# Kernel optimization log

Hardware: AMD Instinct MI355X
Metric: run time of the kernel (lower is better)

## Reference

```python
import jax, jax.numpy as jnp
import numpy as np

B, P, D, A = 256, 196, 512, 512

def setup_inputs() -> dict:
    key = jax.random.key(0)
    ks = jax.random.split(key, 12)
    sc = 1.0 / np.sqrt(D)
    sa = 1.0 / np.sqrt(A)
    return {
        "encoder_out": jax.random.normal(ks[0], (B, P, D), jnp.float32),
        "decoder_hidden": jax.random.normal(ks[1], (B, D), jnp.float32),
        "st": jax.random.normal(ks[2], (B, D), jnp.float32),
        "Wv": jax.random.normal(ks[3], (D, A), jnp.float32) * sc,
        "bv": jnp.zeros((A,), jnp.float32),
        "Wh": jax.random.normal(ks[4], (D, A), jnp.float32) * sc,
        "bh": jnp.zeros((A,), jnp.float32),
        "Ws": jax.random.normal(ks[5], (D, A), jnp.float32) * sc,
        "bs": jnp.zeros((A,), jnp.float32),
        "Wav": jax.random.normal(ks[6], (A,), jnp.float32) * sa,
        "bav": jnp.zeros((), jnp.float32),
        "Was": jax.random.normal(ks[7], (A,), jnp.float32) * sa,
        "bas": jnp.zeros((), jnp.float32),
    }

def reference(encoder_out, decoder_hidden, st, Wv, bv, Wh, bh, Ws, bs, Wav, bav, Was, bas):
    # hidden: (B, A)
    hidden = decoder_hidden @ Wh + bh
    # v: (B, P, A)
    v = jnp.einsum('bpd,da->bpa', encoder_out, Wv) + bv
    # z_t: (B, P) -- additive attention scores over pixels
    z_t = jnp.einsum('bpa,a->bp', jnp.tanh(v + hidden[:, None, :]), Wav) + bav
    alpha_t = jax.nn.softmax(z_t, axis=1)
    # c_t: (B, D) -- attention-weighted encoding
    c_t = jnp.einsum('bpd,bp->bd', encoder_out, alpha_t)
    # sentinel branch: s (B, A), s_att (B, 1)
    s = st @ Ws + bs
    s_att = jnp.tanh(s + hidden) @ Was + bas  # (B,)
    z_t_extended = jnp.concatenate([z_t, s_att[:, None]], axis=1)  # (B, P+1)
    alpha_t_hat = jax.nn.softmax(z_t_extended, axis=1)
    beta_t = alpha_t_hat[:, -1:]  # (B, 1)
    c_hat_t = beta_t * st + (1.0 - beta_t) * c_t
    return (c_hat_t, alpha_t, beta_t)
```

## Files before the change

kernel.cpp:

```cpp
#include <hip/hip_runtime.h>
#include <hip/hip_bf16.h>
#include <cstdint>

#define B_ 256
#define P_ 196
#define D_ 512
#define A_ 512

#define OUT_CHAT  0
#define OUT_ALPHA (B_*D_)
#define OUT_BETA  (B_*D_ + B_*P_)

typedef unsigned short ushort_t;
typedef uint32_t u32;
typedef uint64_t u64;
typedef __attribute__((ext_vector_type(8))) __bf16 bf16x8;
typedef __attribute__((ext_vector_type(4))) float f32x4;

__device__ __forceinline__ ushort_t f2bf(float f) {
    union { float f; u32 i; } v; v.f = f;
    u32 r = (v.i + 0x7fffu + ((v.i >> 16) & 1u)) >> 16;
    return (ushort_t)r;
}
__device__ __forceinline__ float bfbits2f(u32 lo16) {
    union { u32 i; float f; } v; v.i = lo16 << 16; return v.f;
}
__device__ __forceinline__ u32 cvt2bf(float x, float y) {
    union { __hip_bfloat162 h; u32 u; } v;
    v.h = __float22bfloat162_rn(make_float2(x, y));
    return v.u;
}
__device__ __forceinline__ float tanh_fast(float x) {
    float e = __expf(2.0f * x);
    return 1.0f - 2.0f / (e + 1.0f);
}
__device__ __forceinline__ void async_load16(const ushort_t* g, ushort_t* l) {
    __builtin_amdgcn_global_load_lds(
        (const __attribute__((address_space(1))) unsigned int*)g,
        (__attribute__((address_space(3))) unsigned int*)l, 16, 0, 0);
}

__global__ __launch_bounds__(256) void k_prep(
    const float* __restrict__ E, const float* __restrict__ dh,
    const float* __restrict__ st,
    const float* __restrict__ Wv, const float* __restrict__ Wh,
    const float* __restrict__ Ws,
    ushort_t* __restrict__ Ebf, ushort_t* __restrict__ dhbf,
    ushort_t* __restrict__ stbf,
    ushort_t* __restrict__ WvT, ushort_t* __restrict__ WhT,
    ushort_t* __restrict__ WsT)
{
    __shared__ ushort_t tile[32][33];
    int bx = blockIdx.x;
    if (bx < 12544) {
        size_t i0 = (size_t)bx * 512 + threadIdx.x;
        const float4* src = (const float4*)E;
        u64* dst = (u64*)Ebf;
        float4 v0 = src[i0];
        float4 v1 = src[i0 + 256];
        dst[i0]       = (u64)cvt2bf(v0.x, v0.y) | ((u64)cvt2bf(v0.z, v0.w) << 32);
        dst[i0 + 256] = (u64)cvt2bf(v1.x, v1.y) | ((u64)cvt2bf(v1.z, v1.w) << 32);
    } else if (bx < 12672) {
        int gid = (bx - 12544) * 256 + threadIdx.x;
        float4 dv = ((const float4*)dh)[gid];
        float4 sv = ((const float4*)st)[gid];
        ((u64*)dhbf)[gid] = (u64)cvt2bf(dv.x, dv.y) | ((u64)cvt2bf(dv.z, dv.w) << 32);
        ((u64*)stbf)[gid] = (u64)cvt2bf(sv.x, sv.y) | ((u64)cvt2bf(sv.z, sv.w) << 32);
    } else {
        int idx = bx - 12672;
        int z   = idx >> 8;
        int rem = idx & 255;
        int tby = rem >> 4, tbx = rem & 15;
        const float* W  = (z == 0) ? Wv  : (z == 1) ? Wh  : Ws;
        ushort_t*    WT = (z == 0) ? WvT : (z == 1) ? WhT : WsT;
        int t = threadIdx.x, r = t >> 5, c = t & 31;
#pragma unroll
        for (int i = 0; i < 4; ++i) {
            int row = r + 8 * i;
            tile[row][c] = f2bf(W[(size_t)(tby * 32 + row) * A_ + tbx * 32 + c]);
        }
        __syncthreads();
#pragma unroll
        for (int i = 0; i < 4; ++i) {
            int row = r + 8 * i;
            WT[(size_t)(tbx * 32 + row) * D_ + tby * 32 + c] = tile[c][row];
        }
    }
}

#define PADK 72

__global__ __launch_bounds__(256) void k1_mfma(
    const ushort_t* __restrict__ dhbf, const ushort_t* __restrict__ stbf,
    const ushort_t* __restrict__ WhT,  const ushort_t* __restrict__ WsT,
    const float* __restrict__ bh, const float* __restrict__ bs,
    float* __restrict__ hidden_ws, float* __restrict__ s_ws)
{
    __shared__ ushort_t As[128 * PADK];
    __shared__ ushort_t Bs[128 * PADK];

    int mat = blockIdx.z;
    const ushort_t* Abf = mat ? stbf : dhbf;
    const ushort_t* WT  = mat ? WsT  : WhT;
    const float*    bia = mat ? bs   : bh;
    float*          outp = mat ? s_ws : hidden_ws;

    int tid = threadIdx.x;
    int m0 = blockIdx.y * 128;
    int n0 = blockIdx.x * 128;

    int lane = tid & 63, w = tid >> 6;
    int wm = w & 1, wn = w >> 1;
    int col = lane & 15, q = lane >> 4;

    f32x4 acc[4][4];
#pragma unroll
    for (int tm = 0; tm < 4; ++tm)
#pragma unroll
        for (int tn = 0; tn < 4; ++tn)
            acc[tm][tn] = (f32x4){0.f, 0.f, 0.f, 0.f};

    const ushort_t* arow = As + (wm * 64 + col) * PADK + q * 8;
    const ushort_t* brow = Bs + (wn * 64 + col) * PADK + q * 8;

    int sr = tid >> 3, sc = tid & 7;
    for (int kt = 0; kt < D_ / 64; ++kt) {
#pragma unroll
        for (int i = 0; i < 4; ++i) {
            int row = sr + i * 32;
            *(uint4*)(As + row * PADK + sc * 8) =
                *(const uint4*)(Abf + (size_t)(m0 + row) * D_ + kt * 64 + sc * 8);
            *(uint4*)(Bs + row * PADK + sc * 8) =
                *(const uint4*)(WT + (size_t)(n0 + row) * D_ + kt * 64 + sc * 8);
        }
        __syncthreads();
#pragma unroll
        for (int ks = 0; ks < 2; ++ks) {
            bf16x8 afr[4];
#pragma unroll
            for (int tm = 0; tm < 4; ++tm)
                afr[tm] = *(const bf16x8*)(arow + tm * 16 * PADK + ks * 32);
#pragma unroll
            for (int tn = 0; tn < 4; ++tn) {
                bf16x8 bfr = *(const bf16x8*)(brow + tn * 16 * PADK + ks * 32);
#pragma unroll
                for (int tm = 0; tm < 4; ++tm)
                    acc[tm][tn] = __builtin_amdgcn_mfma_f32_16x16x32_bf16(
                        afr[tm], bfr, acc[tm][tn], 0, 0, 0);
            }
        }
        __syncthreads();
    }

#pragma unroll
    for (int tm = 0; tm < 4; ++tm)
#pragma unroll
        for (int r = 0; r < 4; ++r) {
            int b = m0 + wm * 64 + tm * 16 + q * 4 + r;
#pragma unroll
            for (int tn = 0; tn < 4; ++tn) {
                int n = n0 + wn * 64 + tn * 16 + col;
                outp[(size_t)b * A_ + n] = acc[tm][tn][r] + bia[n];
            }
        }
}

#define BM 128
#define BN 256
#define BKk 64
__global__ __launch_bounds__(256, 3) void k2_z_bf(
    const ushort_t* __restrict__ Ebf, const ushort_t* __restrict__ WvT,
    const float* __restrict__ hidden_ws, const float* __restrict__ bv,
    const float* __restrict__ Wav, float* __restrict__ z2_ws)
{
    __shared__ ushort_t As[BM * BKk];
    __shared__ ushort_t Bs[BN * BKk];
    __shared__ float hv_s[2][BN];
    __shared__ float wav_s[BN];
    __shared__ float zpart[2][BM];

    int tid = threadIdx.x;
    int m0  = blockIdx.x * BM;
    int n0  = blockIdx.y * BN;
    int b0  = m0 / P_;
    int b1  = (m0 + BM - 1) / P_;

    {
        int a = n0 + tid;
        float bva = bv[a];
        hv_s[0][tid] = hidden_ws[(size_t)b0 * A_ + a] + bva;
        hv_s[1][tid] = hidden_ws[(size_t)b1 * A_ + a] + bva;
        wav_s[tid]   = Wav[a];
    }

    int lane = tid & 63, w = tid >> 6;
    int wm = w & 1, wn = w >> 1;
    int col = lane & 15, q = lane >> 4;

    f32x4 acc[4][8];
#pragma unroll
    for (int tm = 0; tm < 4; ++tm)
#pragma unroll
        for (int tn = 0; tn < 8; ++tn)
            acc[tm][tn] = (f32x4){0.f, 0.f, 0.f, 0.f};

    int srow = tid >> 3, spos = tid & 7;
    int gch  = spos ^ (srow & 7);
    const ushort_t* agb = Ebf + (size_t)(m0 + srow) * D_ + gch * 8;
    const ushort_t* bgb = WvT + (size_t)(n0 + srow) * D_ + gch * 8;
    ushort_t* alb = As + tid * 8;
    ushort_t* blb = Bs + tid * 8;

    int fx = col & 7;

    for (int kt = 0; kt < D_ / BKk; ++kt) {
#pragma unroll
        for (int i = 0; i < 4; ++i)
            async_load16(agb + (size_t)i * 32 * D_ + kt * BKk, alb + i * 2048);
#pragma unroll
        for (int i = 0; i < 8; ++i)
            async_load16(bgb + (size_t)i * 32 * D_ + kt * BKk, blb + i * 2048);
        __syncthreads();
#pragma unroll
        for (int ks = 0; ks < 2; ++ks) {
            bf16x8 afr[4];
#pragma unroll
            for (int tm = 0; tm < 4; ++tm)
                afr[tm] = *(const bf16x8*)(As + (wm * 64 + tm * 16 + col) * BKk
                                              + (((ks * 4 + q) ^ fx) * 8));
#pragma unroll
            for (int tn = 0; tn < 8; ++tn) {
                bf16x8 bfr = *(const bf16x8*)(Bs + (wn * 128 + tn * 16 + col) * BKk
                                                 + (((ks * 4 + q) ^ fx) * 8));
#pragma unroll
                for (int tm = 0; tm < 4; ++tm)
                    acc[tm][tn] = __builtin_amdgcn_mfma_f32_16x16x32_bf16(
                        afr[tm], bfr, acc[tm][tn], 0, 0, 0);
            }
        }
        __syncthreads();
    }

#pragma unroll
    for (int tm = 0; tm < 4; ++tm) {
#pragma unroll
        for (int r = 0; r < 4; ++r) {
            int row = wm * 64 + tm * 16 + q * 4 + r;
            int m   = m0 + row;
            int bsel = (m / P_) - b0;
            float zr = 0.f;
#pragma unroll
            for (int tn = 0; tn < 8; ++tn) {
                int nl = wn * 128 + tn * 16 + col;
                zr += wav_s[nl] * tanh_fast(acc[tm][tn][r] + hv_s[bsel][nl]);
            }
#pragma unroll
            for (int msk = 1; msk < 16; msk <<= 1)
                zr += __shfl_xor(zr, msk, 64);
            if (col == 0) zpart[wn][row] = zr;
        }
    }
    __syncthreads();
    if (tid < BM)
        z2_ws[(size_t)blockIdx.y * (B_ * P_) + m0 + tid] =
            zpart[0][tid] + zpart[1][tid];
}

__global__ __launch_bounds__(256) void k3_softmax(
    const float* __restrict__ z2_ws, const float* __restrict__ hidden_ws,
    const float* __restrict__ s_ws, const float* __restrict__ Was,
    const float* __restrict__ bas, const float* __restrict__ bav,
    float* __restrict__ alpha_ws, float* __restrict__ beta_ws,
    float* __restrict__ out)
{
    __shared__ float red[4];
    __shared__ float bm_s, bl_s, sa_s;
    int b = blockIdx.x, t = threadIdx.x;

    {
        int a0 = t, a1 = t + 256;
        float part = Was[a0] * tanh_fast(s_ws[(size_t)b * A_ + a0] + hidden_ws[(size_t)b * A_ + a0])
                   + Was[a1] * tanh_fast(s_ws[(size_t)b * A_ + a1] + hidden_ws[(size_t)b * A_ + a1]);
#pragma unroll
        for (int o = 32; o >= 1; o >>= 1) part += __shfl_down(part, o, 64);
        if ((t & 63) == 0) red[t >> 6] = part;
        __syncthreads();
        if (t == 0) sa_s = red[0] + red[1] + red[2] + red[3] + bas[0];
        __syncthreads();
    }

    float zv = (t < P_) ? (z2_ws[(size_t)b * P_ + t]
                         + z2_ws[(size_t)(B_ * P_) + (size_t)b * P_ + t] + bav[0])
                        : -1e30f;

    float m = zv;
#pragma unroll
    for (int o = 32; o >= 1; o >>= 1) m = fmaxf(m, __shfl_xor(m, o, 64));
    if ((t & 63) == 0) red[t >> 6] = m;
    __syncthreads();
    if (t == 0) bm_s = fmaxf(fmaxf(red[0], red[1]), fmaxf(red[2], red[3]));
    __syncthreads();
    float m1 = bm_s;

    float e = (t < P_) ? __expf(zv - m1) : 0.f;
    float s = e;
#pragma unroll
    for (int o = 32; o >= 1; o >>= 1) s += __shfl_xor(s, o, 64);
    if ((t & 63) == 0) red[t >> 6] = s;
    __syncthreads();
    if (t == 0) bl_s = red[0] + red[1] + red[2] + red[3];
    __syncthreads();
    float l1 = bl_s;

    if (t < P_) {
        float alpha = e / l1;
        alpha_ws[(size_t)b * P_ + t] = alpha;
        out[OUT_ALPHA + (size_t)b * P_ + t] = alpha;
    }
    float sa = sa_s;
    float m2 = fmaxf(m1, sa);
    float l2 = __expf(m1 - m2) * l1 + __expf(sa - m2);
    float beta = __expf(sa - m2) / l2;
    if (t == 0) {
        beta_ws[b] = beta;
        out[OUT_BETA + b] = beta;
    }
}

__global__ __launch_bounds__(256) void k4_final(
    const ushort_t* __restrict__ Ebf, const float* __restrict__ st,
    const float* __restrict__ alpha_ws, const float* __restrict__ beta_ws,
    float* __restrict__ out)
{
    __shared__ float al[P_];
    int b = blockIdx.x, t = threadIdx.x;
    if (t < P_) al[t] = alpha_ws[(size_t)b * P_ + t];
    __syncthreads();
    const u32* eb = (const u32*)(Ebf + (size_t)b * P_ * D_) + t;
    float a0 = 0.f, a1 = 0.f;
#pragma unroll 4
    for (int p = 0; p < P_; ++p) {
        u32 u = eb[(size_t)p * (D_ / 2)];
        float ap = al[p];
        a0 = fmaf(ap, bfbits2f(u & 0xffffu), a0);
        a1 = fmaf(ap, bfbits2f(u >> 16), a1);
    }
    float beta = beta_ws[b];
    float2 su = *(const float2*)(st + (size_t)b * D_ + 2 * t);
    float c0 = beta * su.x + (1.f - beta) * a0;
    float c1 = beta * su.y + (1.f - beta) * a1;
    *(float2*)(out + (size_t)b * D_ + 2 * t) = make_float2(c0, c1);
}

extern "C" void kernel_launch(void* const* d_in, const int* in_sizes, int n_in,
                              void* d_out, int out_size, void* d_ws, size_t ws_size,
                              hipStream_t stream)
{
    (void)in_sizes; (void)n_in; (void)out_size; (void)ws_size;
    const float* E   = (const float*)d_in[0];
    const float* dh  = (const float*)d_in[1];
    const float* st  = (const float*)d_in[2];
    const float* Wv  = (const float*)d_in[3];
    const float* bv  = (const float*)d_in[4];
    const float* Wh  = (const float*)d_in[5];
    const float* bh  = (const float*)d_in[6];
    const float* Ws  = (const float*)d_in[7];
    const float* bs  = (const float*)d_in[8];
    const float* Wav = (const float*)d_in[9];
    const float* bav = (const float*)d_in[10];
    const float* Was = (const float*)d_in[11];
    const float* bas = (const float*)d_in[12];
    float* out = (float*)d_out;

    char* ws = (char*)d_ws;
    ushort_t* WvT     = (ushort_t*)(ws);
    ushort_t* WhT     = (ushort_t*)(ws + 524288);
    ushort_t* WsT     = (ushort_t*)(ws + 1048576);
    float*    alpha_w = (float*)(ws + 1572864);
    float*    beta_w  = (float*)(ws + 1773568);
    float*    z2_w    = (float*)(ws + 1774592);
    ushort_t* dhbf    = (ushort_t*)(ws + 2176000);
    ushort_t* stbf    = (ushort_t*)(ws + 2438144);
    float*    hidden_w= (float*)(ws + 2700288);
    float*    s_w     = (float*)(ws + 3224576);
    ushort_t* Ebf     = (ushort_t*)(ws + 3748864);

    k_prep<<<12544 + 128 + 768, 256, 0, stream>>>(E, dh, st, Wv, Wh, Ws,
                                                  Ebf, dhbf, stbf, WvT, WhT, WsT);
    k1_mfma<<<dim3(4, 2, 2), 256, 0, stream>>>(dhbf, stbf, WhT, WsT, bh, bs,
                                               hidden_w, s_w);
    k2_z_bf<<<dim3((B_ * P_) / BM, A_ / BN), 256, 0, stream>>>(
        Ebf, WvT, hidden_w, bv, Wav, z2_w);
    k3_softmax<<<256, 256, 0, stream>>>(z2_w, hidden_w, s_w, Was, bas, bav,
                                        alpha_w, beta_w, out);
    k4_final<<<256, 256, 0, stream>>>(Ebf, st, alpha_w, beta_w, out);
}
```

Baseline: 258.0 us.

## Double-buffer K tiles in the z-score GEMM to overlap loads with MFMA

Halves the K tile to 32 and adds two LDS buffers so the async loads for the next K slice are issued while MFMAs run on the current one. The first tile is prefetched before the loop, and the swizzle is adapted to the 4-chunk row width. This is meant to hide global-to-LDS latency that the single-buffered load-sync-compute-sync loop exposed. The cost is twice as many iterations with smaller compute per barrier. Keeping the same LDS footprint preserves occupancy at 3 blocks per CU.

```diff
diff --git a/kernel.cpp b/kernel.cpp
--- a/kernel.cpp
+++ b/kernel.cpp
@@ -167,14 +167,14 @@
 
 #define BM 128
 #define BN 256
-#define BKk 64
+#define BKp 32
 __global__ __launch_bounds__(256, 3) void k2_z_bf(
     const ushort_t* __restrict__ Ebf, const ushort_t* __restrict__ WvT,
     const float* __restrict__ hidden_ws, const float* __restrict__ bv,
     const float* __restrict__ Wav, float* __restrict__ z2_ws)
 {
-    __shared__ ushort_t As[BM * BKk];
-    __shared__ ushort_t Bs[BN * BKk];
+    __shared__ ushort_t As[2][BM * BKp];
+    __shared__ ushort_t Bs[2][BN * BKp];
     __shared__ float hv_s[2][BN];
     __shared__ float wav_s[BN];
     __shared__ float zpart[2][BM];
@@ -185,58 +185,65 @@
     int b0  = m0 / P_;
     int b1  = (m0 + BM - 1) / P_;
 
+    int srow = tid >> 2, spos = tid & 3;
+    int gch  = spos ^ (srow & 3);
+    const ushort_t* agb = Ebf + (size_t)(m0 + srow) * D_ + gch * 8;
+    const ushort_t* bgb = WvT + (size_t)(n0 + srow) * D_ + gch * 8;
+
+    int lane = tid & 63, w = tid >> 6;
+    int wm = w & 1, wn = w >> 1;
+    int col = lane & 15, q = lane >> 4;
+    int fx = col & 3;
+
+    f32x4 acc[4][8];
+#pragma unroll
+    for (int tm = 0; tm < 4; ++tm)
+#pragma unroll
+        for (int tn = 0; tn < 8; ++tn)
+            acc[tm][tn] = (f32x4){0.f, 0.f, 0.f, 0.f};
+
     {
+#pragma unroll
+        for (int i = 0; i < 2; ++i)
+            async_load16(agb + (size_t)i * 64 * D_, &As[0][tid * 8 + i * 2048]);
+#pragma unroll
+        for (int i = 0; i < 4; ++i)
+            async_load16(bgb + (size_t)i * 64 * D_, &Bs[0][tid * 8 + i * 2048]);
         int a = n0 + tid;
         float bva = bv[a];
         hv_s[0][tid] = hidden_ws[(size_t)b0 * A_ + a] + bva;
         hv_s[1][tid] = hidden_ws[(size_t)b1 * A_ + a] + bva;
         wav_s[tid]   = Wav[a];
     }
-
-    int lane = tid & 63, w = tid >> 6;
-    int wm = w & 1, wn = w >> 1;
-    int col = lane & 15, q = lane >> 4;
-
-    f32x4 acc[4][8];
-#pragma unroll
-    for (int tm = 0; tm < 4; ++tm)
-#pragma unroll
-        for (int tn = 0; tn < 8; ++tn)
-            acc[tm][tn] = (f32x4){0.f, 0.f, 0.f, 0.f};
-
-    int srow = tid >> 3, spos = tid & 7;
-    int gch  = spos ^ (srow & 7);
-    const ushort_t* agb = Ebf + (size_t)(m0 + srow) * D_ + gch * 8;
-    const ushort_t* bgb = WvT + (size_t)(n0 + srow) * D_ + gch * 8;
-    ushort_t* alb = As + tid * 8;
-    ushort_t* blb = Bs + tid * 8;
-
-    int fx = col & 7;
-
-    for (int kt = 0; kt < D_ / BKk; ++kt) {
-#pragma unroll
-        for (int i = 0; i < 4; ++i)
-            async_load16(agb + (size_t)i * 32 * D_ + kt * BKk, alb + i * 2048);
-#pragma unroll
-        for (int i = 0; i < 8; ++i)
-            async_load16(bgb + (size_t)i * 32 * D_ + kt * BKk, blb + i * 2048);
-        __syncthreads();
-#pragma unroll
-        for (int ks = 0; ks < 2; ++ks) {
-            bf16x8 afr[4];
+    __syncthreads();
+
+#pragma unroll
+    for (int kt = 0; kt < 16; ++kt) {
+        int cb = kt & 1;
+        if (kt < 15) {
+            int nb = cb ^ 1;
+#pragma unroll
+            for (int i = 0; i < 2; ++i)
+                async_load16(agb + (size_t)i * 64 * D_ + (kt + 1) * BKp,
+                             &As[nb][tid * 8 + i * 2048]);
+#pragma unroll
+            for (int i = 0; i < 4; ++i)
+                async_load16(bgb + (size_t)i * 64 * D_ + (kt + 1) * BKp,
+                             &Bs[nb][tid * 8 + i * 2048]);
+        }
+        bf16x8 afr[4];
+#pragma unroll
+        for (int tm = 0; tm < 4; ++tm)
+            afr[tm] = *(const bf16x8*)(&As[cb][(wm * 64 + tm * 16 + col) * BKp
+                                              + ((q ^ fx) * 8)]);
+#pragma unroll
+        for (int tn = 0; tn < 8; ++tn) {
+            bf16x8 bfr = *(const bf16x8*)(&Bs[cb][(wn * 128 + tn * 16 + col) * BKp
+                                                  + ((q ^ fx) * 8)]);
 #pragma unroll
             for (int tm = 0; tm < 4; ++tm)
-                afr[tm] = *(const bf16x8*)(As + (wm * 64 + tm * 16 + col) * BKk
-                                              + (((ks * 4 + q) ^ fx) * 8));
-#pragma unroll
-            for (int tn = 0; tn < 8; ++tn) {
-                bf16x8 bfr = *(const bf16x8*)(Bs + (wn * 128 + tn * 16 + col) * BKk
-                                                 + (((ks * 4 + q) ^ fx) * 8));
-#pragma unroll
-                for (int tm = 0; tm < 4; ++tm)
-                    acc[tm][tn] = __builtin_amdgcn_mfma_f32_16x16x32_bf16(
-                        afr[tm], bfr, acc[tm][tn], 0, 0, 0);
-            }
+                acc[tm][tn] = __builtin_amdgcn_mfma_f32_16x16x32_bf16(
+                    afr[tm], bfr, acc[tm][tn], 0, 0, 0);
         }
         __syncthreads();
     }
```

New measurement: 276.2 us. 7.0% more time.
